# Performance work log

Measured on AMD Instinct MI355X. Metric: run time of the kernel, lower is better.

## Reference

```python
import jax, jax.numpy as jnp
import numpy as np

K_NN = 32          # configs['k']
LEAKY_ALPHA = 0.2  # configs['alpha']
NHEADS = 8         # all heads share gat_W0/gat_a0 in the weights dict -> tiled output
NEG_INF = -9e15    # masked-softmax fill used by dense GAT


@jax.custom_vjp
def grad_reverse(x):
    # GradientReversalLayer: identity forward, negated gradient backward
    return x

def _gr_fwd(x):
    return x, None

def _gr_bwd(res, g):
    return (-g,)

grad_reverse.defvjp(_gr_fwd, _gr_bwd)


def setup_inputs() -> dict:
    key = jax.random.key(0)
    ks = jax.random.split(key, 11)
    N, D = 6144, 512           # N = (num_domains+1)*batch_size = 4*1536
    H1, H2, G = 256, 128, 64   # hidden_layers=[256,128], gat_hidden=[64]
    C, ND = 16, 3              # num_classes, num source-domain discriminators

    def xav(k, shape):
        limit = np.float32(np.sqrt(6.0 / (shape[0] + shape[1])) * 1.414)
        return jax.random.uniform(k, shape, jnp.float32, -limit, limit)

    return {
        "x": jax.random.normal(ks[0], (N, D), jnp.float32),
        "fc_W0": xav(ks[1], (D, H1)),
        "fc_b0": jax.random.normal(ks[2], (H1,), jnp.float32) * 0.01,
        "fc_W1": xav(ks[3], (H1, H2)),
        "fc_b1": jax.random.normal(ks[4], (H2,), jnp.float32) * 0.01,
        "gat_W": xav(ks[5], (H2, G)),
        "gat_a": jax.random.normal(ks[6], (2 * G, 1), jnp.float32) * 0.1,
        "cls_W": xav(ks[7], (NHEADS * G, C)),
        "cls_b": jax.random.normal(ks[8], (C,), jnp.float32) * 0.01,
        "dsc_W": jax.random.uniform(ks[9], (ND, NHEADS * G, 2), jnp.float32),
        "dsc_b": jax.random.uniform(ks[10], (ND, 2), jnp.float32),
    }


def reference(x, fc_W0, fc_b0, fc_W1, fc_b1, gat_W, gat_a, cls_W, cls_b, dsc_W, dsc_b):
    # --- feature extractor MLP (Linear 'fc' + relu), dropout=0 / eval mode ---
    h = jax.nn.relu(x @ fc_W0 + fc_b0)
    h = jax.nn.relu(h @ fc_W1 + fc_b1)          # [N, 128]
    n = h.shape[0]

    # --- AdjacencyLayer / DistanceLayer: kNN over pairwise L2 distances ---
    sq = jnp.sum(h * h, axis=1)
    d2 = sq[:, None] + sq[None, :] - 2.0 * (h @ h.T)      # [N, N] squared dists
    d2 = d2 + jnp.eye(n, dtype=h.dtype) * 1e9             # exclude self from kNN
    _, idx = jax.lax.top_k(-jax.lax.stop_gradient(d2), K_NN)  # [N, K]
    adj = jnp.zeros((n, n), h.dtype).at[jnp.arange(n)[:, None], idx].set(1.0)
    adj = adj + jnp.eye(n, dtype=h.dtype)                 # self loops

    # --- dense GraphAttentionLayer (single shared head, tiled nheads times) ---
    Wh = h @ gat_W                                        # [N, G]
    Gd = Wh.shape[1]
    f1 = Wh @ gat_a[:Gd]                                  # [N, 1]
    f2 = Wh @ gat_a[Gd:]                                  # [N, 1]
    e = jax.nn.leaky_relu(f1 + f2.T, LEAKY_ALPHA)         # [N, N]
    att = jax.nn.softmax(jnp.where(adj > 0, e, NEG_INF), axis=1)
    hp = jax.nn.elu(att @ Wh)                             # [N, G]
    gat_out = jnp.tile(hp, (1, NHEADS))                   # concat of shared heads

    # --- class head + domain discriminators behind gradient reversal ---
    cls_logits = gat_out @ cls_W + cls_b                  # [N, C]
    rev = grad_reverse(gat_out)
    dsc_logits = jnp.einsum('nd,kdo->nko', rev, dsc_W) + dsc_b  # [N, ND, 2]
    return jnp.concatenate([cls_logits, dsc_logits.reshape(n, -1)], axis=1)
```

## Files before the change

### kernel.cpp

```cpp
#include <hip/hip_runtime.h>
#include <float.h>

#define N_PTS 6144
#define D_IN  512
#define H1_DIM 256
#define H2_DIM 128
#define G_DIM  64
#define KNN    32
#define NOUT   22

typedef short s8v __attribute__((ext_vector_type(8)));
typedef float f32x4 __attribute__((ext_vector_type(4)));
typedef unsigned u32x4 __attribute__((ext_vector_type(4)));
typedef unsigned short u16;
typedef unsigned long long u64;

__device__ __forceinline__ u16 f2bf(float f) {
  unsigned u = __float_as_uint(f);
  u += 0x7FFFu + ((u >> 16) & 1u);
  return (u16)(u >> 16);
}
__device__ __forceinline__ float bf2f(u16 s) {
  return __uint_as_float(((unsigned)s) << 16);
}
__device__ __forceinline__ void split3(float v, u16& a0, u16& a1, u16& a2) {
  a0 = f2bf(v);
  float r1 = v - bf2f(a0);
  a1 = f2bf(r1);
  a2 = f2bf(r1 - bf2f(a1));
}

template<int BM, bool AF32, bool SPLITK, bool BIAS, bool RELU, bool WF32, bool WSPLIT, bool WKEY>
__global__ __launch_bounds__(256, 4) void mfma_gemm(
    const void* __restrict__ A0any, const u16* __restrict__ A1_, const u16* __restrict__ A2_,
    const u16* __restrict__ B0_, const u16* __restrict__ B1_, const u16* __restrict__ B2_,
    const float* __restrict__ bias,
    float* __restrict__ Cf, u16* __restrict__ C0, u16* __restrict__ C1, u16* __restrict__ C2,
    int Ktot, int Ks, int ldC, size_t MN, int rowoff)
{
  const int MT = BM / 32, NT = 2;
  __shared__ u16 lds[(BM + 64) * 32 * 3];
  u16* Ap[3] = { lds, lds + BM * 32, lds + 2 * BM * 32 };
  u16* Bp[3] = { lds + 3 * BM * 32, lds + 3 * BM * 32 + 2048, lds + 3 * BM * 32 + 4096 };

  const int t = threadIdx.x;
  const int lane = t & 63, wave = t >> 6;
  const int wm = wave >> 1, wn = wave & 1;
  const int m0 = blockIdx.y * BM, n0 = blockIdx.x * 64;
  const int kz = blockIdx.z * Ks;

  f32x4 acc[MT][NT] = {};

  for (int k0 = 0; k0 < Ks; k0 += 32) {
    if (k0) __syncthreads();
    const int kb = kz + k0;
    if (AF32) {
      const float* A = (const float*)A0any;
      #pragma unroll
      for (int c0 = 0; c0 < BM * 4; c0 += 256) {
        int c = c0 + t;
        int row = c >> 2, slot = c & 3;
        const float* g = A + (size_t)(m0 + row) * Ktot + kb + slot * 8;
        f32x4 fa = *(const f32x4*)g;
        f32x4 fb = *(const f32x4*)(g + 4);
        int dst = row * 32 + ((slot ^ ((row >> 1) & 3)) << 3);
        s8v v0, v1, v2;
        #pragma unroll
        for (int e = 0; e < 4; ++e) {
          u16 a0, a1, a2; split3(fa[e], a0, a1, a2);
          v0[e] = (short)a0; v1[e] = (short)a1; v2[e] = (short)a2;
        }
        #pragma unroll
        for (int e = 0; e < 4; ++e) {
          u16 a0, a1, a2; split3(fb[e], a0, a1, a2);
          v0[4 + e] = (short)a0; v1[4 + e] = (short)a1; v2[4 + e] = (short)a2;
        }
        *(s8v*)(Ap[0] + dst) = v0;
        *(s8v*)(Ap[1] + dst) = v1;
        *(s8v*)(Ap[2] + dst) = v2;
      }
    } else {
      const u16* As[3] = { (const u16*)A0any, A1_, A2_ };
      #pragma unroll
      for (int c0 = 0; c0 < BM * 4; c0 += 256) {
        int c = c0 + t;
        int row = c >> 2, slot = c & 3;
        size_t g = (size_t)(m0 + row) * Ktot + kb + slot * 8;
        int dst = row * 32 + ((slot ^ ((row >> 1) & 3)) << 3);
        #pragma unroll
        for (int p = 0; p < 3; ++p)
          *(s8v*)(Ap[p] + dst) = *(const s8v*)(As[p] + g);
      }
    }
    {
      const u16* Bs[3] = { B0_, B1_, B2_ };
      int row = t >> 2, slot = t & 3;
      size_t g = (size_t)(n0 + row) * Ktot + kb + slot * 8;
      int dst = row * 32 + ((slot ^ ((row >> 1) & 3)) << 3);
      #pragma unroll
      for (int p = 0; p < 3; ++p)
        *(s8v*)(Bp[p] + dst) = *(const s8v*)(Bs[p] + g);
    }
    __syncthreads();

    s8v af[3][MT], bf[3][NT];
    #pragma unroll
    for (int mt = 0; mt < MT; ++mt) {
      int r = wm * (BM / 2) + mt * 16 + (lane & 15);
      int off = r * 32 + (((lane >> 4) ^ ((r >> 1) & 3)) << 3);
      #pragma unroll
      for (int p = 0; p < 3; ++p) af[p][mt] = *(const s8v*)(Ap[p] + off);
    }
    #pragma unroll
    for (int nt = 0; nt < NT; ++nt) {
      int r = wn * 32 + nt * 16 + (lane & 15);
      int off = r * 32 + (((lane >> 4) ^ ((r >> 1) & 3)) << 3);
      #pragma unroll
      for (int p = 0; p < 3; ++p) bf[p][nt] = *(const s8v*)(Bp[p] + off);
    }
    #pragma unroll
    for (int mt = 0; mt < MT; ++mt)
      #pragma unroll
      for (int nt = 0; nt < NT; ++nt) {
        f32x4 a = acc[mt][nt];
        a = __builtin_amdgcn_mfma_f32_16x16x32_bf16(af[0][mt], bf[0][nt], a, 0, 0, 0);
        a = __builtin_amdgcn_mfma_f32_16x16x32_bf16(af[0][mt], bf[1][nt], a, 0, 0, 0);
        a = __builtin_amdgcn_mfma_f32_16x16x32_bf16(af[1][mt], bf[0][nt], a, 0, 0, 0);
        a = __builtin_amdgcn_mfma_f32_16x16x32_bf16(af[1][mt], bf[1][nt], a, 0, 0, 0);
        a = __builtin_amdgcn_mfma_f32_16x16x32_bf16(af[0][mt], bf[2][nt], a, 0, 0, 0);
        a = __builtin_amdgcn_mfma_f32_16x16x32_bf16(af[2][mt], bf[0][nt], a, 0, 0, 0);
        acc[mt][nt] = a;
      }
  }

  #pragma unroll
  for (int mt = 0; mt < MT; ++mt) {
    #pragma unroll
    for (int nt = 0; nt < NT; ++nt) {
      int col = n0 + wn * 32 + nt * 16 + (lane & 15);
      float bv = (BIAS && !SPLITK) ? bias[col] : 0.f;
      float sqc = WKEY ? bias[col] : 0.f;
      #pragma unroll
      for (int v = 0; v < 4; ++v) {
        int row = m0 + wm * (BM / 2) + mt * 16 + (lane >> 4) * 4 + v;
        float val = acc[mt][nt][v] + bv;
        size_t o = (size_t)row * ldC + col;
        if (SPLITK) {
          Cf[(size_t)blockIdx.z * MN + o] = val;
        } else if (WKEY) {
          float f = fmaf(-2.f, val, sqc);
          unsigned ub = __float_as_uint(f);
          unsigned uu = (ub & 0x80000000u) ? ~ub : (ub | 0x80000000u);
          if (rowoff + row == col) uu = 0xFFFFFFFFu;
          ((unsigned*)Cf)[o] = uu;
        } else {
          if (RELU) val = fmaxf(val, 0.f);
          if (WF32) Cf[o] = val;
          if (WSPLIT) {
            u16 a0, a1, a2; split3(val, a0, a1, a2);
            C0[o] = a0; C1[o] = a1; C2[o] = a2;
          }
        }
      }
    }
  }
}

template<int S, bool BIAS, bool RELU, bool WF32, bool WSPLIT>
__global__ void combine(const float* __restrict__ P, const float* __restrict__ bias,
                        size_t MN, int Ncols,
                        float* __restrict__ Cf, u16* __restrict__ C0,
                        u16* __restrict__ C1, u16* __restrict__ C2)
{
  size_t idx = ((size_t)blockIdx.x * 256 + threadIdx.x) * 4;
  if (idx >= MN) return;
  f32x4 s = *(const f32x4*)(P + idx);
  #pragma unroll
  for (int z = 1; z < S; ++z) s += *(const f32x4*)(P + (size_t)z * MN + idx);
  int n = (int)(idx % (size_t)Ncols);
  #pragma unroll
  for (int e = 0; e < 4; ++e) {
    float v = s[e] + (BIAS ? bias[n + e] : 0.f);
    if (RELU) v = fmaxf(v, 0.f);
    if (WF32) Cf[idx + e] = v;
    if (WSPLIT) {
      u16 a0, a1, a2; split3(v, a0, a1, a2);
      C0[idx + e] = a0; C1[idx + e] = a1; C2[idx + e] = a2;
    }
  }
}

__global__ void trans_split(const float* __restrict__ W, u16* __restrict__ p0,
                            u16* __restrict__ p1, u16* __restrict__ p2, int K, int N)
{
  int id = blockIdx.x * 256 + threadIdx.x;
  if (id >= K * N) return;
  int k = id / N, n = id % N;
  u16 a0, a1, a2;
  split3(W[id], a0, a1, a2);
  size_t o = (size_t)n * K + k;
  p0[o] = a0; p1[o] = a1; p2[o] = a2;
}

__global__ void prep_head(const float* __restrict__ cW, const float* __restrict__ cb,
                          const float* __restrict__ dW, const float* __restrict__ db,
                          float* __restrict__ Wc, float* __restrict__ bc)
{
  int t = threadIdx.x;
  for (int idx = t; idx < 64 * NOUT; idx += 256) {
    int g = idx / NOUT, c = idx % NOUT;
    float s = 0.f;
    if (c < 16) {
      for (int r = 0; r < 8; ++r) s += cW[(r * 64 + g) * 16 + c];
    } else {
      int k = (c - 16) >> 1, o = (c - 16) & 1;
      for (int r = 0; r < 8; ++r) s += dW[k * 1024 + (r * 64 + g) * 2 + o];
    }
    Wc[idx] = s;
  }
  if (t < NOUT) bc[t] = (t < 16) ? cb[t] : db[t - 16];
}

__global__ void row_stats(const float* __restrict__ h, const float* __restrict__ Wh,
                          const float* __restrict__ ga, float* __restrict__ sq,
                          float* __restrict__ f1, float* __restrict__ f2)
{
  int i = blockIdx.x * 256 + threadIdx.x;
  const float* hr = h + (size_t)i * H2_DIM;
  float s = 0.f;
  for (int k = 0; k < H2_DIM; ++k) { float v = hr[k]; s = fmaf(v, v, s); }
  sq[i] = s;
  const float* wr = Wh + (size_t)i * G_DIM;
  float a = 0.f, b = 0.f;
  for (int g = 0; g < G_DIM; ++g) {
    float w = wr[g];
    a = fmaf(w, ga[g], a);
    b = fmaf(w, ga[G_DIM + g], b);
  }
  f1[i] = a; f2[i] = b;
}

__global__ __launch_bounds__(256) void topk_att(const unsigned* __restrict__ Sb,
    const float* __restrict__ f1, const float* __restrict__ f2,
    const float* __restrict__ Wh, const float* __restrict__ Wc, const float* __restrict__ bc,
    float* __restrict__ out, int m0)
{
  const int t = threadIdx.x;
  const int lane = t & 63, wv = t >> 6;
  const int row4 = blockIdx.x * 4 + wv;
  const int i = m0 + row4;
  const unsigned* Srow = Sb + (size_t)row4 * N_PTS;

  __shared__ float WcL[64 * NOUT];
  __shared__ u64 candS[4][256];
  __shared__ int neighS[4][33];
  __shared__ float attS[4][33];
  __shared__ float hpfS[4][64];

  for (int idx = t; idx < 64 * NOUT; idx += 256) WcL[idx] = Wc[idx];
  __syncthreads();

  unsigned q[24];
  #pragma unroll
  for (int c = 0; c < 24; ++c) {
    u32x4 v = *(const u32x4*)(Srow + (c << 8) + (lane << 2));
    unsigned a = v[0] < v[1] ? v[0] : v[1];
    unsigned b = v[2] < v[3] ? v[2] : v[3];
    q[c] = a < b ? a : b;
  }

  unsigned mnl = q[0];
  #pragma unroll
  for (int c = 1; c < 24; ++c) mnl = q[c] < mnl ? q[c] : mnl;
  unsigned mxl = mnl;
  #pragma unroll
  for (int off = 32; off > 0; off >>= 1) {
    unsigned o1 = __shfl_xor(mnl, off); mnl = o1 < mnl ? o1 : mnl;
    unsigned o2 = __shfl_xor(mxl, off); mxl = o2 > mxl ? o2 : mxl;
  }

  long long lo = (long long)mnl - 1, hi = (long long)mxl;
  while (hi - lo > 1) {
    long long span = hi - lo;
    unsigned m1 = (unsigned)(lo + (span >> 2));
    unsigned m2 = (unsigned)(lo + (span >> 1));
    unsigned m3 = (unsigned)(hi - (span >> 2));
    int c1 = 0, c2 = 0, c3 = 0;
    #pragma unroll
    for (int c = 0; c < 24; ++c) {
      c1 += (q[c] <= m1);
      c2 += (q[c] <= m2);
      c3 += (q[c] <= m3);
    }
    #pragma unroll
    for (int off = 32; off > 0; off >>= 1) {
      c1 += __shfl_xor(c1, off);
      c2 += __shfl_xor(c2, off);
      c3 += __shfl_xor(c3, off);
    }
    if (c1 >= KNN)       { hi = m1; }
    else if (c2 >= KNN)  { lo = m1; hi = m2; }
    else if (c3 >= KNN)  { lo = m2; hi = m3; }
    else                 { lo = m3; }
  }
  const unsigned Q = (unsigned)hi;

  candS[wv][lane] = ~0ull;
  candS[wv][64 + lane] = ~0ull;
  const u64 below = (lane == 0) ? 0ull : (~0ull >> (64 - lane));
  int cnt = 0;
  #pragma unroll
  for (int c = 0; c < 24; ++c) {
    bool act = (q[c] <= Q);
    u64 mask = __ballot(act);
    if (act) {
      int pos = cnt + (int)__popcll(mask & below);
      if (pos < 32) {
        u32x4 v = *(const u32x4*)(Srow + (c << 8) + (lane << 2));
        #pragma unroll
        for (int e = 0; e < 4; ++e) {
          int j = (c << 8) + (lane << 2) + e;
          candS[wv][pos * 4 + e] = ((u64)v[e] << 13) | (unsigned)j;
        }
      }
    }
    cnt += (int)__popcll(mask);
  }

  if (cnt <= 32) {
    u64 v0 = candS[wv][2 * lane], v1 = candS[wv][2 * lane + 1];
    const int e0 = 2 * lane, e1 = e0 + 1;
    for (int k = 2; k <= 128; k <<= 1) {
      for (int j = k >> 1; j >= 2; j >>= 1) {
        int half = j >> 1;
        u64 o0 = __shfl_xor(v0, half);
        u64 o1 = __shfl_xor(v1, half);
        bool up0 = ((e0 & k) == 0) == ((e0 & j) == 0);
        bool up1 = ((e1 & k) == 0) == ((e1 & j) == 0);
        v0 = up0 ? (v0 < o0 ? v0 : o0) : (v0 > o0 ? v0 : o0);
        v1 = up1 ? (v1 < o1 ? v1 : o1) : (v1 > o1 ? v1 : o1);
      }
      bool asc = ((e0 & k) == 0);
      u64 a = v0 < v1 ? v0 : v1, b = v0 < v1 ? v1 : v0;
      v0 = asc ? a : b;
      v1 = asc ? b : a;
    }
    if (lane < 16) {
      neighS[wv][2 * lane]     = (int)(v0 & 0x1FFFu);
      neighS[wv][2 * lane + 1] = (int)(v1 & 0x1FFFu);
    }
    if (lane == 0) neighS[wv][32] = i;
  } else {
    candS[wv][128 + lane] = ~0ull;
    candS[wv][192 + lane] = ~0ull;
    int cnt2 = 0;
    #pragma unroll
    for (int c = 0; c < 24; ++c) {
      bool act = (q[c] <= Q);
      u64 mask = __ballot(act);
      if (act) {
        int pos = cnt2 + (int)__popcll(mask & below);
        if (pos < 64) {
          u32x4 v = *(const u32x4*)(Srow + (c << 8) + (lane << 2));
          #pragma unroll
          for (int e = 0; e < 4; ++e) {
            int j = (c << 8) + (lane << 2) + e;
            candS[wv][pos * 4 + e] = ((u64)v[e] << 13) | (unsigned)j;
          }
        }
      }
      cnt2 += (int)__popcll(mask);
    }
    for (int k = 2; k <= 256; k <<= 1) {
      for (int j = k >> 1; j >= 1; j >>= 1) {
        #pragma unroll
        for (int s = 0; s < 4; ++s) {
          int e = lane + s * 64;
          int p = e ^ j;
          if (p > e) {
            u64 a = candS[wv][e], b = candS[wv][p];
            bool asc = ((e & k) == 0);
            if ((a > b) == asc) { candS[wv][e] = b; candS[wv][p] = a; }
          }
        }
      }
    }
    if (lane < KNN) neighS[wv][lane] = (int)(candS[wv][lane] & 0x1FFFu);
    if (lane == 0) neighS[wv][32] = i;
  }

  {
    float e = -FLT_MAX;
    if (lane < 33) {
      float raw = f1[i] + f2[neighS[wv][lane]];
      e = raw > 0.f ? raw : 0.2f * raw;
    }
    float mx = e;
    #pragma unroll
    for (int off = 32; off > 0; off >>= 1) mx = fmaxf(mx, __shfl_xor(mx, off));
    float ex = (lane < 33) ? expf(e - mx) : 0.f;
    float sm = ex;
    #pragma unroll
    for (int off = 32; off > 0; off >>= 1) sm += __shfl_xor(sm, off);
    if (lane < 33) attS[wv][lane] = ex / sm;
  }

  {
    float s = 0.f;
    for (int m = 0; m < 33; ++m)
      s = fmaf(attS[wv][m], Wh[(size_t)neighS[wv][m] * G_DIM + lane], s);
    hpfS[wv][lane] = s > 0.f ? s : expm1f(s);
  }

  if (lane < NOUT) {
    float o = bc[lane];
    for (int g = 0; g < 64; ++g) o = fmaf(hpfS[wv][g], WcL[g * NOUT + lane], o);
    out[(size_t)i * NOUT + lane] = o;
  }
}

extern "C" void kernel_launch(void* const* d_in, const int* in_sizes, int n_in,
                              void* d_out, int out_size, void* d_ws, size_t ws_size,
                              hipStream_t stream)
{
  const float* x  = (const float*)d_in[0];
  const float* W0 = (const float*)d_in[1];
  const float* b0 = (const float*)d_in[2];
  const float* W1 = (const float*)d_in[3];
  const float* b1 = (const float*)d_in[4];
  const float* gW = (const float*)d_in[5];
  const float* ga = (const float*)d_in[6];
  const float* cW = (const float*)d_in[7];
  const float* cb = (const float*)d_in[8];
  const float* dW = (const float*)d_in[9];
  const float* db = (const float*)d_in[10];
  float* out = (float*)d_out;

  char* base = (char*)d_ws;
  char* w = base;
  auto alloc = [&](size_t bytes) { char* p = w; w += (bytes + 255) & ~(size_t)255; return p; };
  u16 *W0p[3], *W1p[3], *gWp[3], *h1p[3], *hp[3];
  for (int p = 0; p < 3; ++p) W0p[p] = (u16*)alloc((size_t)D_IN * H1_DIM * 2);
  for (int p = 0; p < 3; ++p) W1p[p] = (u16*)alloc((size_t)H1_DIM * H2_DIM * 2);
  for (int p = 0; p < 3; ++p) gWp[p] = (u16*)alloc((size_t)H2_DIM * G_DIM * 2);
  for (int p = 0; p < 3; ++p) h1p[p] = (u16*)alloc((size_t)N_PTS * H1_DIM * 2);
  for (int p = 0; p < 3; ++p) hp[p]  = (u16*)alloc((size_t)N_PTS * H2_DIM * 2);
  float* hF  = (float*)alloc((size_t)N_PTS * H2_DIM * 4);
  float* WhF = (float*)alloc((size_t)N_PTS * G_DIM * 4);
  float* sqv = (float*)alloc(N_PTS * 4);
  float* f1v = (float*)alloc(N_PTS * 4);
  float* f2v = (float*)alloc(N_PTS * 4);
  float* Wc  = (float*)alloc(64 * NOUT * 4);
  float* bc  = (float*)alloc(64 * 4);

  char* pbase = w;
  const size_t MN1 = (size_t)N_PTS * H1_DIM;
  const size_t MN2 = (size_t)N_PTS * H2_DIM;
  const size_t MN3 = (size_t)N_PTS * G_DIM;
  float* P1 = (float*)alloc(4 * MN1 * 4);
  float* P2 = (float*)alloc(4 * MN2 * 4);
  float* P3 = (float*)alloc(4 * MN3 * 4);
  float* Sb = (float*)pbase;

  size_t used_persist = (size_t)(pbase - base);
  size_t avail = (ws_size > used_persist) ? (ws_size - used_persist) / 4 : 0;
  int rowblk = 128;
  const int rcand[] = {6144, 3072, 1536, 768, 384, 256, 128};
  for (int c : rcand) { if ((size_t)c * N_PTS <= avail) { rowblk = c; break; } }

  trans_split<<<(D_IN * H1_DIM + 255) / 256, 256, 0, stream>>>(W0, W0p[0], W0p[1], W0p[2], D_IN, H1_DIM);
  trans_split<<<(H1_DIM * H2_DIM + 255) / 256, 256, 0, stream>>>(W1, W1p[0], W1p[1], W1p[2], H1_DIM, H2_DIM);
  trans_split<<<(H2_DIM * G_DIM + 255) / 256, 256, 0, stream>>>(gW, gWp[0], gWp[1], gWp[2], H2_DIM, G_DIM);
  prep_head<<<1, 256, 0, stream>>>(cW, cb, dW, db, Wc, bc);

  mfma_gemm<64, true, true, false, false, false, false, false>
      <<<dim3(H1_DIM / 64, N_PTS / 64, 4), 256, 0, stream>>>(
      x, nullptr, nullptr, W0p[0], W0p[1], W0p[2], nullptr,
      P1, nullptr, nullptr, nullptr, D_IN, D_IN / 4, H1_DIM, MN1, 0);
  combine<4, true, true, false, true><<<(int)(MN1 / 1024), 256, 0, stream>>>(
      P1, b0, MN1, H1_DIM, nullptr, h1p[0], h1p[1], h1p[2]);

  mfma_gemm<64, false, true, false, false, false, false, false>
      <<<dim3(H2_DIM / 64, N_PTS / 64, 4), 256, 0, stream>>>(
      h1p[0], h1p[1], h1p[2], W1p[0], W1p[1], W1p[2], nullptr,
      P2, nullptr, nullptr, nullptr, H1_DIM, H1_DIM / 4, H2_DIM, MN2, 0);
  combine<4, true, true, true, true><<<(int)(MN2 / 1024), 256, 0, stream>>>(
      P2, b1, MN2, H2_DIM, hF, hp[0], hp[1], hp[2]);

  mfma_gemm<64, false, true, false, false, false, false, false>
      <<<dim3(G_DIM / 64, N_PTS / 64, 4), 256, 0, stream>>>(
      hp[0], hp[1], hp[2], gWp[0], gWp[1], gWp[2], nullptr,
      P3, nullptr, nullptr, nullptr, H2_DIM, H2_DIM / 4, G_DIM, MN3, 0);
  combine<4, false, false, true, false><<<(int)(MN3 / 1024), 256, 0, stream>>>(
      P3, nullptr, MN3, G_DIM, WhF, nullptr, nullptr, nullptr);

  row_stats<<<N_PTS / 256, 256, 0, stream>>>(hF, WhF, ga, sqv, f1v, f2v);

  for (int b = 0; b < N_PTS / rowblk; ++b) {
    mfma_gemm<128, false, false, false, false, false, false, true>
        <<<dim3(N_PTS / 64, rowblk / 128, 1), 256, 0, stream>>>(
        hp[0] + (size_t)b * rowblk * H2_DIM, hp[1] + (size_t)b * rowblk * H2_DIM,
        hp[2] + (size_t)b * rowblk * H2_DIM, hp[0], hp[1], hp[2], sqv,
        Sb, nullptr, nullptr, nullptr, H2_DIM, H2_DIM, N_PTS, 0, b * rowblk);
    topk_att<<<rowblk / 4, 256, 0, stream>>>((const unsigned*)Sb, f1v, f2v, WhF, Wc, bc, out, b * rowblk);
  }
}
```

Baseline: 187.9 us.

## Pick kNN threshold via bitonic sort of lane minima; merge weight-split launches

```diff
diff --git a/kernel.cpp b/kernel.cpp
--- a/kernel.cpp
+++ b/kernel.cpp
@@ -190,16 +190,25 @@
   }
 }
 
-__global__ void trans_split(const float* __restrict__ W, u16* __restrict__ p0,
-                            u16* __restrict__ p1, u16* __restrict__ p2, int K, int N)
+__global__ void trans_split3(const float* __restrict__ W0, u16* __restrict__ a0,
+                             u16* __restrict__ a1, u16* __restrict__ a2,
+                             const float* __restrict__ W1, u16* __restrict__ b0,
+                             u16* __restrict__ b1, u16* __restrict__ b2,
+                             const float* __restrict__ gW, u16* __restrict__ c0,
+                             u16* __restrict__ c1, u16* __restrict__ c2)
 {
   int id = blockIdx.x * 256 + threadIdx.x;
-  if (id >= K * N) return;
+  const int S0 = D_IN * H1_DIM, S1 = H1_DIM * H2_DIM, S2 = H2_DIM * G_DIM;
+  const float* W; u16 *p0, *p1, *p2; int K, N;
+  if (id < S0)           { W = W0; p0 = a0; p1 = a1; p2 = a2; K = D_IN;   N = H1_DIM; }
+  else if (id < S0 + S1) { id -= S0; W = W1; p0 = b0; p1 = b1; p2 = b2; K = H1_DIM; N = H2_DIM; }
+  else if (id < S0 + S1 + S2) { id -= S0 + S1; W = gW; p0 = c0; p1 = c1; p2 = c2; K = H2_DIM; N = G_DIM; }
+  else return;
   int k = id / N, n = id % N;
-  u16 a0, a1, a2;
-  split3(W[id], a0, a1, a2);
+  u16 x0, x1, x2;
+  split3(W[id], x0, x1, x2);
   size_t o = (size_t)n * K + k;
-  p0[o] = a0; p1[o] = a1; p2[o] = a2;
+  p0[o] = x0; p1[o] = x1; p2[o] = x2;
 }
 
 __global__ void prep_head(const float* __restrict__ cW, const float* __restrict__ cb,
@@ -269,45 +278,27 @@
     q[c] = a < b ? a : b;
   }
 
-  unsigned mnl = q[0];
+  unsigned lmin = q[0];
   #pragma unroll
-  for (int c = 1; c < 24; ++c) mnl = q[c] < mnl ? q[c] : mnl;
-  unsigned mxl = mnl;
-  #pragma unroll
-  for (int off = 32; off > 0; off >>= 1) {
-    unsigned o1 = __shfl_xor(mnl, off); mnl = o1 < mnl ? o1 : mnl;
-    unsigned o2 = __shfl_xor(mxl, off); mxl = o2 > mxl ? o2 : mxl;
-  }
-
-  long long lo = (long long)mnl - 1, hi = (long long)mxl;
-  while (hi - lo > 1) {
-    long long span = hi - lo;
-    unsigned m1 = (unsigned)(lo + (span >> 2));
-    unsigned m2 = (unsigned)(lo + (span >> 1));
-    unsigned m3 = (unsigned)(hi - (span >> 2));
-    int c1 = 0, c2 = 0, c3 = 0;
-    #pragma unroll
-    for (int c = 0; c < 24; ++c) {
-      c1 += (q[c] <= m1);
-      c2 += (q[c] <= m2);
-      c3 += (q[c] <= m3);
-    }
-    #pragma unroll
-    for (int off = 32; off > 0; off >>= 1) {
-      c1 += __shfl_xor(c1, off);
-      c2 += __shfl_xor(c2, off);
-      c3 += __shfl_xor(c3, off);
-    }
-    if (c1 >= KNN)       { hi = m1; }
-    else if (c2 >= KNN)  { lo = m1; hi = m2; }
-    else if (c3 >= KNN)  { lo = m2; hi = m3; }
-    else                 { lo = m3; }
-  }
-  const unsigned Q = (unsigned)hi;
+  for (int c = 1; c < 24; ++c) lmin = q[c] < lmin ? q[c] : lmin;
+
+  unsigned sv = lmin;
+  for (int k = 2; k <= 64; k <<= 1) {
+    for (int j = k >> 1; j >= 1; j >>= 1) {
+      unsigned o = __shfl_xor(sv, j);
+      bool up = ((lane & k) == 0) == ((lane & j) == 0);
+      sv = up ? (sv < o ? sv : o) : (sv > o ? sv : o);
+    }
+  }
+  unsigned Q = __shfl(sv, 31);
+  const unsigned s0 = __shfl(sv, 0);
+
+  const u64 below = (lane == 0) ? 0ull : (~0ull >> (64 - lane));
 
   candS[wv][lane] = ~0ull;
   candS[wv][64 + lane] = ~0ull;
-  const u64 below = (lane == 0) ? 0ull : (~0ull >> (64 - lane));
+  candS[wv][128 + lane] = ~0ull;
+  candS[wv][192 + lane] = ~0ull;
   int cnt = 0;
   #pragma unroll
   for (int c = 0; c < 24; ++c) {
@@ -315,7 +306,7 @@
     u64 mask = __ballot(act);
     if (act) {
       int pos = cnt + (int)__popcll(mask & below);
-      if (pos < 32) {
+      if (pos < 64) {
         u32x4 v = *(const u32x4*)(Srow + (c << 8) + (lane << 2));
         #pragma unroll
         for (int e = 0; e < 4; ++e) {
@@ -325,6 +316,56 @@
       }
     }
     cnt += (int)__popcll(mask);
+  }
+
+  if (cnt > 64) {
+    long long lo = (long long)s0 - 1, hi = (long long)Q;
+    while (hi - lo > 1) {
+      long long span = hi - lo;
+      unsigned m1 = (unsigned)(lo + (span >> 2));
+      unsigned m2 = (unsigned)(lo + (span >> 1));
+      unsigned m3 = (unsigned)(hi - (span >> 2));
+      int c1 = 0, c2 = 0, c3 = 0;
+      #pragma unroll
+      for (int c = 0; c < 24; ++c) {
+        c1 += (q[c] <= m1);
+        c2 += (q[c] <= m2);
+        c3 += (q[c] <= m3);
+      }
+      #pragma unroll
+      for (int off = 32; off > 0; off >>= 1) {
+        c1 += __shfl_xor(c1, off);
+        c2 += __shfl_xor(c2, off);
+        c3 += __shfl_xor(c3, off);
+      }
+      if (c1 >= KNN)       { hi = m1; }
+      else if (c2 >= KNN)  { lo = m1; hi = m2; }
+      else if (c3 >= KNN)  { lo = m2; hi = m3; }
+      else                 { lo = m3; }
+    }
+    Q = (unsigned)hi;
+    candS[wv][lane] = ~0ull;
+    candS[wv][64 + lane] = ~0ull;
+    candS[wv][128 + lane] = ~0ull;
+    candS[wv][192 + lane] = ~0ull;
+    cnt = 0;
+    #pragma unroll
+    for (int c = 0; c < 24; ++c) {
+      bool act = (q[c] <= Q);
+      u64 mask = __ballot(act);
+      if (act) {
+        int pos = cnt + (int)__popcll(mask & below);
+        if (pos < 64) {
+          u32x4 v = *(const u32x4*)(Srow + (c << 8) + (lane << 2));
+          #pragma unroll
+          for (int e = 0; e < 4; ++e) {
+            int j = (c << 8) + (lane << 2) + e;
+            candS[wv][pos * 4 + e] = ((u64)v[e] << 13) | (unsigned)j;
+          }
+        }
+      }
+      cnt += (int)__popcll(mask);
+    }
   }
 
   if (cnt <= 32) {
@@ -351,26 +392,6 @@
     }
     if (lane == 0) neighS[wv][32] = i;
   } else {
-    candS[wv][128 + lane] = ~0ull;
-    candS[wv][192 + lane] = ~0ull;
-    int cnt2 = 0;
-    #pragma unroll
-    for (int c = 0; c < 24; ++c) {
-      bool act = (q[c] <= Q);
-      u64 mask = __ballot(act);
-      if (act) {
-        int pos = cnt2 + (int)__popcll(mask & below);
-        if (pos < 64) {
-          u32x4 v = *(const u32x4*)(Srow + (c << 8) + (lane << 2));
-          #pragma unroll
-          for (int e = 0; e < 4; ++e) {
-            int j = (c << 8) + (lane << 2) + e;
-            candS[wv][pos * 4 + e] = ((u64)v[e] << 13) | (unsigned)j;
-          }
-        }
-      }
-      cnt2 += (int)__popcll(mask);
-    }
     for (int k = 2; k <= 256; k <<= 1) {
       for (int j = k >> 1; j >= 1; j >>= 1) {
         #pragma unroll
@@ -468,9 +489,9 @@
   const int rcand[] = {6144, 3072, 1536, 768, 384, 256, 128};
   for (int c : rcand) { if ((size_t)c * N_PTS <= avail) { rowblk = c; break; } }
 
-  trans_split<<<(D_IN * H1_DIM + 255) / 256, 256, 0, stream>>>(W0, W0p[0], W0p[1], W0p[2], D_IN, H1_DIM);
-  trans_split<<<(H1_DIM * H2_DIM + 255) / 256, 256, 0, stream>>>(W1, W1p[0], W1p[1], W1p[2], H1_DIM, H2_DIM);
-  trans_split<<<(H2_DIM * G_DIM + 255) / 256, 256, 0, stream>>>(gW, gWp[0], gWp[1], gWp[2], H2_DIM, G_DIM);
+  const int TS = D_IN * H1_DIM + H1_DIM * H2_DIM + H2_DIM * G_DIM;
+  trans_split3<<<(TS + 255) / 256, 256, 0, stream>>>(
+      W0, W0p[0], W0p[1], W0p[2], W1, W1p[0], W1p[1], W1p[2], gW, gWp[0], gWp[1], gWp[2]);
   prep_head<<<1, 256, 0, stream>>>(cW, cb, dW, db, Wc, bc);
 
   mfma_gemm<64, true, true, false, false, false, false, false>
```

New measurement: 190.0 us. Within noise of the previous version (+1.1%).
